# Optimization experiments

Measured on AMD Instinct MI355X. Metric: run time of the kernel, lower is better.

Reference implementation:

```python
import jax, jax.numpy as jnp
import numpy as np


def setup_inputs() -> dict:
    key = jax.random.key(0)
    k1, k2 = jax.random.split(key)
    B, D, H, W = 32, 64, 32, 32
    K = 1024
    z_e = jax.random.normal(k1, (B, D, H, W), dtype=jnp.float32)
    # original init: uniform(-1/K, 1/K); use same scale
    emb = jax.random.uniform(k2, (K, D), dtype=jnp.float32, minval=-1.0 / K, maxval=1.0 / K)
    return {"z_e": z_e, "emb": emb}


COMMITMENT_COST = 0.25


def reference(z_e, emb):
    # z_e: [B, D, H, W], emb: [K, D]
    B, D, H, W = z_e.shape
    K = emb.shape[0]
    z = jnp.transpose(z_e, (0, 2, 3, 1))           # [B, H, W, D]
    flat = z.reshape(-1, D)                        # [N, D]
    N = flat.shape[0]

    dist = (
        jnp.sum(flat * flat, axis=1, keepdims=True)
        + jnp.sum(emb * emb, axis=1)
        - 2.0 * flat @ emb.T
    )
    idx = jnp.argmin(dist, axis=1)                 # [N]
    encodings = jax.nn.one_hot(idx, K, dtype=flat.dtype)  # [N, K]
    z_q = (encodings @ emb).reshape(z.shape)       # [B, H, W, D]

    e_latent_loss = jnp.mean((jax.lax.stop_gradient(z_q) - z) ** 2)
    q_latent_loss = jnp.mean((z_q - jax.lax.stop_gradient(z)) ** 2)
    loss = q_latent_loss + COMMITMENT_COST * e_latent_loss

    # straight-through estimator
    z_st = z + jax.lax.stop_gradient(z_q - z)

    avg_probs = jnp.sum(encodings, axis=0) / jnp.float32(N)
    perplexity = jnp.exp(-jnp.sum(avg_probs * jnp.log(avg_probs + 1e-10)))

    return (jnp.transpose(z_st, (0, 3, 1, 2)), loss, perplexity, encodings)
```

## Files before the change

### kernel.cpp

```cpp
#include <hip/hip_runtime.h>
#include <stdint.h>
#include <math.h>

constexpr int Kk  = 1024;

constexpr int OUT0_N   = 32 * 64 * 1024;
constexpr int OUT_LOSS = OUT0_N;
constexpr int OUT_PERP = OUT0_N + 1;
constexpr int OUT_ENC  = OUT0_N + 2;

constexpr size_t WS_CNT = 0;
constexpr size_t WS_LP  = 4096;
constexpr size_t WS_BN  = 12288;
constexpr size_t WS_MBN = 16384;
constexpr size_t WS_KEY = 16416;

typedef short bf16x8 __attribute__((ext_vector_type(8)));
typedef float f32x16 __attribute__((ext_vector_type(16)));

__device__ __forceinline__ float norm64v(const float4* __restrict__ p) {
#pragma clang fp contract(off)
    float tt[64];
#pragma unroll
    for (int q = 0; q < 16; ++q) {
        float4 v = p[q];
        tt[4 * q + 0] = v.x * v.x;
        tt[4 * q + 1] = v.y * v.y;
        tt[4 * q + 2] = v.z * v.z;
        tt[4 * q + 3] = v.w * v.w;
    }
    float r[8];
#pragma unroll
    for (int j = 0; j < 8; ++j) r[j] = tt[j];
#pragma unroll
    for (int i = 8; i < 64; i += 8)
#pragma unroll
        for (int j = 0; j < 8; ++j) r[j] += tt[i + j];
    return ((r[0] + r[1]) + (r[2] + r[3])) + ((r[4] + r[5]) + (r[6] + r[7]));
}

__device__ __forceinline__ uint32_t fsort(float f) {
    uint32_t b = __float_as_uint(f);
    return (b & 0x80000000u) ? ~b : (b | 0x80000000u);
}

__device__ __forceinline__ unsigned short f2bf(float f) {
    uint32_t u = __float_as_uint(f);
    uint32_t r = (u + 0x7fffu + ((u >> 16) & 1u)) >> 16;
    return (unsigned short)r;
}

__device__ __forceinline__ unsigned long long
exact_key_bn(float A, const float* __restrict__ xr, const float* __restrict__ emb,
             const float* __restrict__ Bn_g, uint32_t code) {
    const float* er = emb + (size_t)code * 64;
    float C = 0.f;
#pragma unroll
    for (int d = 0; d < 64; ++d) C = __builtin_fmaf(xr[d], er[d], C);
    float s = A + Bn_g[code];
    float dist = __builtin_fmaf(-2.f, C, s);
    return ((unsigned long long)fsort(dist) << 32) | code;
}

__global__ __launch_bounds__(256)
void norms_kernel(const float* __restrict__ emb, float* __restrict__ Bn_g,
                  float* __restrict__ maxbn, uint32_t* __restrict__ counts) {
    __shared__ float wred[4];
    const int t = threadIdx.x, lane = t & 63, wv = t >> 6;
    const int code = blockIdx.x * 256 + t;
    float nn = norm64v((const float4*)(emb + (size_t)code * 64));
    Bn_g[code] = nn;
    if (blockIdx.x == 0) ((uint4*)counts)[t] = make_uint4(0u, 0u, 0u, 0u);
    float mx = nn;
#pragma unroll
    for (int m = 1; m < 64; m <<= 1) mx = fmaxf(mx, __shfl_xor(mx, m, 64));
    if (lane == 0) wred[wv] = mx;
    __syncthreads();
    if (t == 0)   maxbn[blockIdx.x * 2 + 0] = fmaxf(wred[0], wred[1]);
    if (t == 128) maxbn[blockIdx.x * 2 + 1] = fmaxf(wred[2], wred[3]);
}

__global__ __launch_bounds__(256, 4)
void dist_mfma(const float* __restrict__ z_e, const float* __restrict__ emb,
               const float* __restrict__ Bn_g, const float* __restrict__ maxbn,
               unsigned long long* __restrict__ lockey, float* __restrict__ out) {
    __shared__ unsigned short ebf[128 * 64];
    __shared__ float Bn_s[128];
    const int t = threadIdx.x, lane = t & 63, wv = t >> 6, g = lane >> 5;
    const int rg = blockIdx.x >> 3, cg = blockIdx.x & 7;
    const int n0 = rg * 128, b = n0 >> 10, hw0 = n0 & 1023;
    const float* zb = z_e + (size_t)b * 65536 + hw0;

    {
        const float4* ep = (const float4*)(emb + (size_t)cg * 8192);
#pragma unroll
        for (int it = 0; it < 8; ++it) {
            int j = t + it * 256;
            float4 v = ep[j];
            int code = j >> 4, q = j & 15;
            ushort4 bv;
            bv.x = f2bf(v.x); bv.y = f2bf(v.y); bv.z = f2bf(v.z); bv.w = f2bf(v.w);
            *(ushort4*)((char*)ebf + code * 128 + ((q * 8) ^ ((code & 7) << 4))) = bv;
        }
    }
    if (t < 128) Bn_s[t] = Bn_g[cg * 128 + t];

    const int rowl = wv * 32 + (lane & 31);
    float xsq = 0.f;
    bf16x8 bfr[4];
#pragma unroll
    for (int s = 0; s < 4; ++s) {
        bf16x8 f;
#pragma unroll
        for (int e = 0; e < 8; ++e) {
            int d = s * 16 + g * 8 + e;
            float x = zb[(size_t)d * 1024 + rowl];
            xsq = __builtin_fmaf(x, x, xsq);
            f[e] = (short)f2bf(x);
        }
        bfr[s] = f;
    }
    xsq += __shfl_xor(xsq, 32, 64);
    const float margin = 0.017f * sqrtf(xsq * maxbn[cg]) + 1.0e-4f;
    __syncthreads();

    const int swz = (lane & 7) << 4;
    const char* ebase = (const char*)ebf + (lane & 31) * 128;

    float4* encz = (float4*)(out + OUT_ENC) + (size_t)blockIdx.x * 4096;
    const float4 zero4 = make_float4(0.f, 0.f, 0.f, 0.f);

    float runmin = 3.4e38f;
#pragma unroll 1
    for (int tm = 0; tm < 4; ++tm) {
        encz[(size_t)(tm * 2 + 0) * 256 + t] = zero4;
        encz[(size_t)(tm * 2 + 1) * 256 + t] = zero4;
        const char* p = ebase + tm * 4096;
        f32x16 acc = {};
#pragma unroll
        for (int s = 0; s < 4; ++s)
            acc = __builtin_amdgcn_mfma_f32_32x32x16_bf16(
                *(const bf16x8*)(p + ((s * 32 + g * 16) ^ swz)), bfr[s], acc, 0, 0, 0);
#pragma unroll
        for (int r = 0; r < 16; ++r) {
            int cl = tm * 32 + (r & 3) + 8 * (r >> 2) + 4 * g;
            runmin = fminf(runmin, __builtin_fmaf(-2.f, acc[r], Bn_s[cl]));
        }
    }
    runmin = fminf(runmin, __shfl_xor(runmin, 32, 64));
    const float thr = runmin + margin;

    uint32_t cnt = 0, c0 = 0, c1 = 0, c2 = 0;
#pragma unroll 1
    for (int tm = 0; tm < 4; ++tm) {
        encz[(size_t)(8 + tm * 2 + 0) * 256 + t] = zero4;
        encz[(size_t)(8 + tm * 2 + 1) * 256 + t] = zero4;
        const char* p = ebase + tm * 4096;
        f32x16 acc = {};
#pragma unroll
        for (int s = 0; s < 4; ++s)
            acc = __builtin_amdgcn_mfma_f32_32x32x16_bf16(
                *(const bf16x8*)(p + ((s * 32 + g * 16) ^ swz)), bfr[s], acc, 0, 0, 0);
#pragma unroll
        for (int r = 0; r < 16; ++r) {
            int cl = tm * 32 + (r & 3) + 8 * (r >> 2) + 4 * g;
            float sv = __builtin_fmaf(-2.f, acc[r], Bn_s[cl]);
            if (sv <= thr) {
                uint32_t gc = (uint32_t)(cg * 128 + cl);
                if (cnt == 0u) c0 = gc; else if (cnt == 1u) c1 = gc; else if (cnt == 2u) c2 = gc;
                ++cnt;
            }
        }
    }
    uint32_t pc = __shfl_xor(cnt, 32, 64);
    uint32_t p0 = __shfl_xor(c0, 32, 64);
    uint32_t p1 = __shfl_xor(c1, 32, 64);
    uint32_t p2 = __shfl_xor(c2, 32, 64);
    if (lane < 32) {
        uint32_t tot = cnt + pc;
        uint32_t lo;
        if (tot > 3u || tot == 0u) {
            lo = 3u << 30;
        } else {
            uint32_t a0 = c0, a1 = c1, a2 = c2;
            if (cnt == 0u)      { a0 = p0; a1 = p1; a2 = p2; }
            else if (cnt == 1u) { a1 = p0; a2 = p1; }
            else if (cnt == 2u) { a2 = p0; }
            if (tot < 2u) a1 = 0u;
            if (tot < 3u) a2 = 0u;
            lo = ((tot - 1u) << 30) | (a0 & 1023u) | ((a1 & 1023u) << 10) | ((a2 & 1023u) << 20);
        }
        unsigned long long key = ((unsigned long long)__float_as_uint(runmin) << 32) | lo;
        lockey[(size_t)(n0 + rowl) * 8 + cg] = key;
    }
}

__global__ __launch_bounds__(256)
void finish_kernel(const float* __restrict__ z_e, const float* __restrict__ emb,
                   const unsigned long long* __restrict__ lockey,
                   const float* __restrict__ Bn_g,
                   const float* __restrict__ maxbn,
                   uint32_t* __restrict__ counts, double* __restrict__ lp,
                   float* __restrict__ out) {
    __shared__ float zs[32 * 68];
    __shared__ float arow[32];
    __shared__ uint32_t scode[32];
    __shared__ uint8_t ncarr[32];
    __shared__ unsigned long long pkey[32][6];
    __shared__ uint32_t pairbuf[192];
    __shared__ uint32_t ovfbuf[32];
    __shared__ uint32_t npairs, novf;
    __shared__ float mbg_s;
    __shared__ unsigned long long rbuf[4];
    __shared__ double lred[4];
    const int t = threadIdx.x, lane = t & 63, wv = t >> 6;
    const int n0 = blockIdx.x * 32;
    const int b = n0 >> 10, hw0 = n0 & 1023;
    const int hwi = t & 31, dg = t >> 5;
    const size_t base = (size_t)b * 65536 + (size_t)(dg * 8) * 1024 + hw0 + hwi;

    if (t == 0) {
        npairs = 0u; novf = 0u;
        float mb = maxbn[0];
#pragma unroll
        for (int i = 1; i < 8; ++i) mb = fmaxf(mb, maxbn[i]);
        mbg_s = mb;
    }

    float zreg[8];
#pragma unroll
    for (int k = 0; k < 8; ++k) zreg[k] = z_e[base + (size_t)k * 1024];
#pragma unroll
    for (int m = 0; m < 2; ++m)
        *(float4*)&zs[hwi * 68 + dg * 8 + 4 * m] =
            make_float4(zreg[4 * m], zreg[4 * m + 1], zreg[4 * m + 2], zreg[4 * m + 3]);
    __syncthreads();

    if (t < 32) {
        const unsigned long long* k8 = lockey + (size_t)(n0 + t) * 8;
        unsigned long long kws[8];
#pragma unroll
        for (int i = 0; i < 8; ++i) kws[i] = k8[i];
        float gmin = 3.4e38f;
#pragma unroll
        for (int i = 0; i < 8; ++i)
            gmin = fminf(gmin, __uint_as_float((uint32_t)(kws[i] >> 32)));
        float A = norm64v((const float4*)&zs[t * 68]);
        arow[t] = A;
        const float thr = gmin + 0.017f * sqrtf(A * mbg_s) + 1.0e-4f;

        int nc = 0; uint32_t cand[6]; bool ovf = false;
#pragma unroll
        for (int i = 0; i < 8; ++i) {
            float f = __uint_as_float((uint32_t)(kws[i] >> 32));
            if (f > thr) continue;
            uint32_t lo = (uint32_t)kws[i], cc = lo >> 30;
            if (cc == 3u) { ovf = true; }
            else {
#pragma unroll
                for (uint32_t q = 0; q < 3u; ++q)
                    if (q <= cc) {
                        if (nc < 6) cand[nc] = (lo >> (10u * q)) & 1023u;
                        ++nc;
                    }
            }
        }
        if (ovf || nc > 6 || nc == 0) {
            ncarr[t] = 255u;
            ovfbuf[atomicAdd(&novf, 1u)] = (uint32_t)t;
        } else if (nc == 1) {
            ncarr[t] = 1u;
            scode[t] = cand[0];
        } else {
            ncarr[t] = (uint8_t)nc;
            uint32_t bs = atomicAdd(&npairs, (uint32_t)nc);
#pragma unroll
            for (int q = 0; q < 6; ++q)
                if (q < nc)
                    pairbuf[bs + q] = ((uint32_t)t << 13) | ((uint32_t)q << 10) | cand[q];
        }
    }
    __syncthreads();

    for (uint32_t p = t; p < npairs; p += 256u) {
        uint32_t pk = pairbuf[p];
        int row = (int)(pk >> 13), slot = (int)((pk >> 10) & 7u);
        pkey[row][slot] = exact_key_bn(arow[row], &zs[row * 68], emb, Bn_g, pk & 1023u);
    }
    __syncthreads();

    for (uint32_t o = 0; o < novf; ++o) {
        int row = (int)ovfbuf[o];
        const float* xr = &zs[row * 68];
        float A = arow[row];
        unsigned long long best = ~0ULL;
#pragma unroll 1
        for (int cq = 0; cq < 4; ++cq) {
            unsigned long long key = exact_key_bn(A, xr, emb, Bn_g, (uint32_t)(t + cq * 256));
            best = (key < best) ? key : best;
        }
#pragma unroll
        for (int m = 1; m < 64; m <<= 1) {
            unsigned long long ok = __shfl_xor(best, m, 64);
            best = (ok < best) ? ok : best;
        }
        if (lane == 0) rbuf[wv] = best;
        __syncthreads();
        if (t == 0) {
            unsigned long long bb = rbuf[0];
#pragma unroll
            for (int w = 1; w < 4; ++w) bb = (rbuf[w] < bb) ? rbuf[w] : bb;
            scode[row] = (uint32_t)bb;
        }
        __syncthreads();
    }

    if (t < 32) {
        uint8_t nc = ncarr[t];
        if (nc >= 2u && nc != 255u) {
            unsigned long long bb = pkey[t][0];
#pragma unroll
            for (int q = 1; q < 6; ++q)
                if (q < (int)nc && pkey[t][q] < bb) bb = pkey[t][q];
            scode[t] = (uint32_t)bb;
        }
    }
    __syncthreads();

    if (t < 32) {
        uint32_t code = scode[t];
        atomicAdd(&counts[code], 1u);
        out[(size_t)OUT_ENC + (size_t)(n0 + t) * 1024 + code] = 1.0f;
    }

    {
        const uint32_t code = scode[hwi];
        const float4* er4 = (const float4*)(emb + (size_t)code * 64) + dg * 2;
        double ls = 0.0;
#pragma unroll
        for (int k4 = 0; k4 < 2; ++k4) {
            float4 e4 = er4[k4];
            float f0 = e4.x, f1 = e4.y, f2 = e4.z, f3 = e4.w;
            size_t off = base + (size_t)(k4 * 4) * 1024;
            {
                float z = zreg[k4 * 4 + 0]; float tt = f0 - z;
                out[off] = z + tt;              ls += (double)tt * (double)tt;
            }
            {
                float z = zreg[k4 * 4 + 1]; float tt = f1 - z;
                out[off + 1024] = z + tt;       ls += (double)tt * (double)tt;
            }
            {
                float z = zreg[k4 * 4 + 2]; float tt = f2 - z;
                out[off + 2048] = z + tt;       ls += (double)tt * (double)tt;
            }
            {
                float z = zreg[k4 * 4 + 3]; float tt = f3 - z;
                out[off + 3072] = z + tt;       ls += (double)tt * (double)tt;
            }
        }
#pragma unroll
        for (int m = 32; m >= 1; m >>= 1) ls += __shfl_down(ls, m, 64);
        if ((t & 63) == 0) lred[t >> 6] = ls;
    }
    __syncthreads();
    if (t == 0) lp[blockIdx.x] = lred[0] + lred[1] + lred[2] + lred[3];
}

__global__ void scalar_kernel(const uint32_t* __restrict__ counts,
                              const double* __restrict__ lp,
                              float* __restrict__ out) {
    __shared__ double redl[4], redh[4];
    const int t = threadIdx.x;
    double ls = 0.0;
    for (int i = t; i < 1024; i += 256) ls += lp[i];
    double h = 0.0;
    for (int i = t; i < Kk; i += 256) {
        double p = (double)counts[i] * (1.0 / 32768.0);
        h += p * log(p + 1e-10);
    }
#pragma unroll
    for (int m = 32; m >= 1; m >>= 1) { ls += __shfl_down(ls, m, 64); h += __shfl_down(h, m, 64); }
    if ((t & 63) == 0) { redl[t >> 6] = ls; redh[t >> 6] = h; }
    __syncthreads();
    if (t == 0) {
        double L = redl[0] + redl[1] + redl[2] + redl[3];
        double H = redh[0] + redh[1] + redh[2] + redh[3];
        out[OUT_PERP] = (float)exp(-H);
        float m32 = (float)(L * (1.0 / 2097152.0));
        out[OUT_LOSS] = m32 + 0.25f * m32;
    }
}

extern "C" void kernel_launch(void* const* d_in, const int* in_sizes, int n_in,
                              void* d_out, int out_size, void* d_ws, size_t ws_size,
                              hipStream_t stream) {
    const float* z_e = (const float*)d_in[0];
    const float* emb = (const float*)d_in[1];
    float* out = (float*)d_out;
    char* ws = (char*)d_ws;

    uint32_t* counts = (uint32_t*)(ws + WS_CNT);
    double*   lp     = (double*)(ws + WS_LP);
    float*    Bn_g   = (float*)(ws + WS_BN);
    float*    mbn    = (float*)(ws + WS_MBN);
    unsigned long long* lockey = (unsigned long long*)(ws + WS_KEY);

    norms_kernel<<<4, 256, 0, stream>>>(emb, Bn_g, mbn, counts);
    dist_mfma<<<2048, 256, 0, stream>>>(z_e, emb, Bn_g, mbn, lockey, out);
    finish_kernel<<<1024, 256, 0, stream>>>(z_e, emb, lockey, Bn_g, mbn, counts, lp, out);
    scalar_kernel<<<1, 256, 0, stream>>>(counts, lp, out);
}
```

Before: 197.1 us.

## Pre-swizzle bf16 codebook once, narrow overflow rescans to flagged column groups

```diff
diff --git a/kernel.cpp b/kernel.cpp
--- a/kernel.cpp
+++ b/kernel.cpp
@@ -13,7 +13,8 @@
 constexpr size_t WS_LP  = 4096;
 constexpr size_t WS_BN  = 12288;
 constexpr size_t WS_MBN = 16384;
-constexpr size_t WS_KEY = 16416;
+constexpr size_t WS_EBF = 20480;
+constexpr size_t WS_KEY = 151552;
 
 typedef short bf16x8 __attribute__((ext_vector_type(8)));
 typedef float f32x16 __attribute__((ext_vector_type(16)));
@@ -53,10 +54,18 @@
 __device__ __forceinline__ unsigned long long
 exact_key_bn(float A, const float* __restrict__ xr, const float* __restrict__ emb,
              const float* __restrict__ Bn_g, uint32_t code) {
-    const float* er = emb + (size_t)code * 64;
+    const float4* e4 = (const float4*)(emb + (size_t)code * 64);
+    float4 ev[16];
+#pragma unroll
+    for (int q = 0; q < 16; ++q) ev[q] = e4[q];
     float C = 0.f;
 #pragma unroll
-    for (int d = 0; d < 64; ++d) C = __builtin_fmaf(xr[d], er[d], C);
+    for (int q = 0; q < 16; ++q) {
+        C = __builtin_fmaf(xr[4 * q + 0], ev[q].x, C);
+        C = __builtin_fmaf(xr[4 * q + 1], ev[q].y, C);
+        C = __builtin_fmaf(xr[4 * q + 2], ev[q].z, C);
+        C = __builtin_fmaf(xr[4 * q + 3], ev[q].w, C);
+    }
     float s = A + Bn_g[code];
     float dist = __builtin_fmaf(-2.f, C, s);
     return ((unsigned long long)fsort(dist) << 32) | code;
@@ -64,13 +73,27 @@
 
 __global__ __launch_bounds__(256)
 void norms_kernel(const float* __restrict__ emb, float* __restrict__ Bn_g,
-                  float* __restrict__ maxbn, uint32_t* __restrict__ counts) {
+                  float* __restrict__ maxbn, uint32_t* __restrict__ counts,
+                  unsigned char* __restrict__ ebf16g) {
     __shared__ float wred[4];
     const int t = threadIdx.x, lane = t & 63, wv = t >> 6;
     const int code = blockIdx.x * 256 + t;
     float nn = norm64v((const float4*)(emb + (size_t)code * 64));
     Bn_g[code] = nn;
     if (blockIdx.x == 0) ((uint4*)counts)[t] = make_uint4(0u, 0u, 0u, 0u);
+
+    {
+        unsigned char* base = ebf16g + (size_t)(code >> 7) * 16384 + (size_t)(code & 127) * 128;
+        const int swz = (code & 7) << 4;
+        const float4* e4 = (const float4*)(emb + (size_t)code * 64);
+#pragma unroll
+        for (int q = 0; q < 16; ++q) {
+            float4 v = e4[q];
+            ushort4 bv;
+            bv.x = f2bf(v.x); bv.y = f2bf(v.y); bv.z = f2bf(v.z); bv.w = f2bf(v.w);
+            *(ushort4*)(base + ((q * 8) ^ swz)) = bv;
+        }
+    }
     float mx = nn;
 #pragma unroll
     for (int m = 1; m < 64; m <<= 1) mx = fmaxf(mx, __shfl_xor(mx, m, 64));
@@ -80,8 +103,9 @@
     if (t == 128) maxbn[blockIdx.x * 2 + 1] = fmaxf(wred[2], wred[3]);
 }
 
-__global__ __launch_bounds__(256, 4)
-void dist_mfma(const float* __restrict__ z_e, const float* __restrict__ emb,
+__global__ __launch_bounds__(256, 5)
+void dist_mfma(const float* __restrict__ z_e,
+               const unsigned char* __restrict__ ebf16g,
                const float* __restrict__ Bn_g, const float* __restrict__ maxbn,
                unsigned long long* __restrict__ lockey, float* __restrict__ out) {
     __shared__ unsigned short ebf[128 * 64];
@@ -92,15 +116,11 @@
     const float* zb = z_e + (size_t)b * 65536 + hw0;
 
     {
-        const float4* ep = (const float4*)(emb + (size_t)cg * 8192);
-#pragma unroll
-        for (int it = 0; it < 8; ++it) {
-            int j = t + it * 256;
-            float4 v = ep[j];
-            int code = j >> 4, q = j & 15;
-            ushort4 bv;
-            bv.x = f2bf(v.x); bv.y = f2bf(v.y); bv.z = f2bf(v.z); bv.w = f2bf(v.w);
-            *(ushort4*)((char*)ebf + code * 128 + ((q * 8) ^ ((code & 7) << 4))) = bv;
+        const float4* ep = (const float4*)(ebf16g + (size_t)cg * 16384);
+#pragma unroll
+        for (int it = 0; it < 4; ++it) {
+            float4 v = ep[it * 256 + t];
+            *(float4*)((char*)ebf + (size_t)(it * 256 + t) * 16) = v;
         }
     }
     if (t < 128) Bn_s[t] = Bn_g[cg * 128 + t];
@@ -206,7 +226,10 @@
     __shared__ float arow[32];
     __shared__ uint32_t scode[32];
     __shared__ uint8_t ncarr[32];
+    __shared__ uint8_t ovfm[32];
+    __shared__ uint8_t ovfnc[32];
     __shared__ unsigned long long pkey[32][6];
+    __shared__ unsigned long long okey[32];
     __shared__ uint32_t pairbuf[192];
     __shared__ uint32_t ovfbuf[32];
     __shared__ uint32_t npairs, novf;
@@ -249,13 +272,13 @@
         arow[t] = A;
         const float thr = gmin + 0.017f * sqrtf(A * mbg_s) + 1.0e-4f;
 
-        int nc = 0; uint32_t cand[6]; bool ovf = false;
+        int nc = 0; uint32_t cand[6]; uint32_t om = 0;
 #pragma unroll
         for (int i = 0; i < 8; ++i) {
             float f = __uint_as_float((uint32_t)(kws[i] >> 32));
             if (f > thr) continue;
             uint32_t lo = (uint32_t)kws[i], cc = lo >> 30;
-            if (cc == 3u) { ovf = true; }
+            if (cc == 3u) { om |= (1u << i); }
             else {
 #pragma unroll
                 for (uint32_t q = 0; q < 3u; ++q)
@@ -265,9 +288,21 @@
                     }
             }
         }
-        if (ovf || nc > 6 || nc == 0) {
+        if (nc > 6 || (nc == 0 && om == 0u)) {
             ncarr[t] = 255u;
             ovfbuf[atomicAdd(&novf, 1u)] = (uint32_t)t;
+        } else if (om) {
+            ncarr[t] = 0u;
+            ovfm[t] = (uint8_t)om;
+            ovfnc[t] = (uint8_t)nc;
+            ovfbuf[atomicAdd(&novf, 1u)] = (uint32_t)t;
+            if (nc > 0) {
+                uint32_t bs = atomicAdd(&npairs, (uint32_t)nc);
+#pragma unroll
+                for (int q = 0; q < 6; ++q)
+                    if (q < nc)
+                        pairbuf[bs + q] = ((uint32_t)t << 13) | ((uint32_t)q << 10) | cand[q];
+            }
         } else if (nc == 1) {
             ncarr[t] = 1u;
             scode[t] = cand[0];
@@ -294,10 +329,21 @@
         const float* xr = &zs[row * 68];
         float A = arow[row];
         unsigned long long best = ~0ULL;
+        if (ncarr[row] == 255u) {
 #pragma unroll 1
-        for (int cq = 0; cq < 4; ++cq) {
-            unsigned long long key = exact_key_bn(A, xr, emb, Bn_g, (uint32_t)(t + cq * 256));
-            best = (key < best) ? key : best;
+            for (int cq = 0; cq < 4; ++cq) {
+                unsigned long long key = exact_key_bn(A, xr, emb, Bn_g, (uint32_t)(t + cq * 256));
+                best = (key < best) ? key : best;
+            }
+        } else {
+            uint32_t om = ovfm[row];
+#pragma unroll 1
+            for (int i = 0; i < 8; ++i) {
+                if ((om & (1u << i)) && t < 128) {
+                    unsigned long long key = exact_key_bn(A, xr, emb, Bn_g, (uint32_t)(i * 128 + t));
+                    best = (key < best) ? key : best;
+                }
+            }
         }
 #pragma unroll
         for (int m = 1; m < 64; m <<= 1) {
@@ -310,18 +356,26 @@
             unsigned long long bb = rbuf[0];
 #pragma unroll
             for (int w = 1; w < 4; ++w) bb = (rbuf[w] < bb) ? rbuf[w] : bb;
-            scode[row] = (uint32_t)bb;
+            if (ncarr[row] == 255u) scode[row] = (uint32_t)bb;
+            else                    okey[row] = bb;
         }
         __syncthreads();
     }
 
     if (t < 32) {
-        uint8_t nc = ncarr[t];
-        if (nc >= 2u && nc != 255u) {
+        uint8_t k = ncarr[t];
+        if (k == 0u) {
+            unsigned long long bb = okey[t];
+            int nc = (int)ovfnc[t];
+#pragma unroll
+            for (int q = 0; q < 6; ++q)
+                if (q < nc && pkey[t][q] < bb) bb = pkey[t][q];
+            scode[t] = (uint32_t)bb;
+        } else if (k >= 2u && k != 255u) {
             unsigned long long bb = pkey[t][0];
 #pragma unroll
             for (int q = 1; q < 6; ++q)
-                if (q < (int)nc && pkey[t][q] < bb) bb = pkey[t][q];
+                if (q < (int)k && pkey[t][q] < bb) bb = pkey[t][q];
             scode[t] = (uint32_t)bb;
         }
     }
@@ -404,10 +458,11 @@
     double*   lp     = (double*)(ws + WS_LP);
     float*    Bn_g   = (float*)(ws + WS_BN);
     float*    mbn    = (float*)(ws + WS_MBN);
+    unsigned char* ebf16g = (unsigned char*)(ws + WS_EBF);
     unsigned long long* lockey = (unsigned long long*)(ws + WS_KEY);
 
-    norms_kernel<<<4, 256, 0, stream>>>(emb, Bn_g, mbn, counts);
-    dist_mfma<<<2048, 256, 0, stream>>>(z_e, emb, Bn_g, mbn, lockey, out);
+    norms_kernel<<<4, 256, 0, stream>>>(emb, Bn_g, mbn, counts, ebf16g);
+    dist_mfma<<<2048, 256, 0, stream>>>(z_e, ebf16g, Bn_g, mbn, lockey, out);
     finish_kernel<<<1024, 256, 0, stream>>>(z_e, emb, lockey, Bn_g, mbn, counts, lp, out);
     scalar_kernel<<<1, 256, 0, stream>>>(counts, lp, out);
 }
```

Result: slower. 202.2 us (+2.6%).
